# Optimization experiments

Measured on AMD Instinct MI355X. Metric: run time of the kernel, lower is better.

The kernel has to match this reference:

```python
import jax, jax.numpy as jnp
import numpy as np

DIM = 768
NUM_HEADS = 12
HEAD_DIM = DIM // NUM_HEADS
EPS = 1e-5


def layer_norm(x, w, b):
    mu = jnp.mean(x, axis=-1, keepdims=True)
    var = jnp.var(x, axis=-1, keepdims=True)
    return (x - mu) * jax.lax.rsqrt(var + EPS) * w + b


def setup_inputs() -> dict:
    key = jax.random.key(0)
    k1, k2, k3, k4, k5, k6, k7 = jax.random.split(key, 7)
    B, N = 8, 1024
    QKV = jax.random.normal(k1, (B, N, 3 * DIM), dtype=jnp.float32)
    q_norm_w = jnp.ones((HEAD_DIM,), jnp.float32)
    q_norm_b = jnp.zeros((HEAD_DIM,), jnp.float32)
    k_norm_w = jnp.ones((HEAD_DIM,), jnp.float32)
    k_norm_b = jnp.zeros((HEAD_DIM,), jnp.float32)
    lim = 1.0 / np.sqrt(DIM)
    proj_w = jax.random.uniform(k2, (DIM, DIM), jnp.float32, -lim, lim)
    proj_b = jax.random.uniform(k3, (DIM,), jnp.float32, -lim, lim)
    return {
        "QKV": QKV,
        "q_norm_w": q_norm_w, "q_norm_b": q_norm_b,
        "k_norm_w": k_norm_w, "k_norm_b": k_norm_b,
        "proj_w": proj_w, "proj_b": proj_b,
    }


def reference(QKV, q_norm_w, q_norm_b, k_norm_w, k_norm_b, proj_w, proj_b):
    B, N, C = QKV.shape
    # (B,N,3,H,D) -> (3,B,H,N,D)
    qkv = QKV.reshape(B, N, 3, NUM_HEADS, HEAD_DIM).transpose(2, 0, 3, 1, 4)
    q, k, v = qkv[0], qkv[1], qkv[2]
    q = layer_norm(q, q_norm_w, q_norm_b)
    k = layer_norm(k, k_norm_w, k_norm_b)
    scale = HEAD_DIM ** (-0.5)
    attn = jnp.einsum('bhnd,bhmd->bhnm', q, k) * scale
    attn = jax.nn.softmax(attn, axis=-1)
    x = jnp.einsum('bhnm,bhmd->bhnd', attn, v)
    x = x.transpose(0, 2, 1, 3).reshape(B, N, DIM)
    # torch Linear: x @ W^T + b
    return jnp.einsum('bnc,dc->bnd', x, proj_w) + proj_b
```

## Files before the change

kernel.cpp:

```cpp
#include <hip/hip_runtime.h>
#include <hip/hip_bf16.h>

#define DIM 768
#define NH 12
#define HD 64
#define B_ 8
#define N_ 1024
#define BH (B_*NH)
#define EPS 1e-5f
#define QSCALE 0.18033688011112042f
#define SMAX 12.0f

typedef short s16x8 __attribute__((ext_vector_type(8)));
typedef float f32x4 __attribute__((ext_vector_type(4)));

__device__ __forceinline__ unsigned pk2bf(float a, float b) {
    __hip_bfloat162 h = __float22bfloat162_rn(float2{a, b});
    union { __hip_bfloat162 h; unsigned u; } cv; cv.h = h;
    return cv.u;
}

__device__ __forceinline__ float fexp2(float x) {
#if __has_builtin(__builtin_amdgcn_exp2f)
    return __builtin_amdgcn_exp2f(x);
#else
    return exp2f(x);
#endif
}

__device__ __forceinline__ void async_cp16(const void* g, void* l) {
    __builtin_amdgcn_global_load_lds(
        (const __attribute__((address_space(1))) unsigned*)g,
        (__attribute__((address_space(3))) unsigned*)l, 16, 0, 0);
}

__global__ __launch_bounds__(256)
void ln_pack_kernel(const float* __restrict__ QKV,
                    const float* __restrict__ qw, const float* __restrict__ qb,
                    const float* __restrict__ kw, const float* __restrict__ kb,
                    unsigned short* __restrict__ Qp,
                    unsigned short* __restrict__ Kp,
                    unsigned short* __restrict__ Vp) {
    int bid = blockIdx.x;
    int bh = bid >> 4, nt = bid & 15;
    int b = bh / NH, h = bh % NH;
    int tid = threadIdx.x, w = tid >> 6, ln = tid & 63;
    int rl = w * 16 + (ln >> 2);
    int part = ln & 3;
    int n = nt * 64 + rl;

    __shared__ __attribute__((aligned(16))) unsigned short vlds[64][72];

    size_t base = ((size_t)(b * N_ + n)) * (3 * DIM) + h * HD + part * 16;
    float4 q[4], k[4], v[4];
    #pragma unroll
    for (int i = 0; i < 4; i++) {
        q[i] = *(const float4*)(QKV + base + i * 4);
        k[i] = *(const float4*)(QKV + base + DIM + i * 4);
        v[i] = *(const float4*)(QKV + base + 2 * DIM + i * 4);
    }

    float s1 = 0.f, s2 = 0.f, t1 = 0.f, t2 = 0.f;
    #pragma unroll
    for (int i = 0; i < 4; i++) {
        s1 += (q[i].x + q[i].y) + (q[i].z + q[i].w);
        s2 += (q[i].x * q[i].x + q[i].y * q[i].y) + (q[i].z * q[i].z + q[i].w * q[i].w);
        t1 += (k[i].x + k[i].y) + (k[i].z + k[i].w);
        t2 += (k[i].x * k[i].x + k[i].y * k[i].y) + (k[i].z * k[i].z + k[i].w * k[i].w);
    }
    #pragma unroll
    for (int m = 1; m < 4; m <<= 1) {
        s1 += __shfl_xor(s1, m, 64);
        s2 += __shfl_xor(s2, m, 64);
        t1 += __shfl_xor(t1, m, 64);
        t2 += __shfl_xor(t2, m, 64);
    }

    int ch = part >> 1;
    size_t tile = (((size_t)bh * 64 + (n >> 4)) * 2 + ch) * 512 + (size_t)(n & 15) * 32 + (part & 1) * 16;

    {
        float mu = s1 * (1.0f / 64.0f);
        float var = s2 * (1.0f / 64.0f) - mu * mu;
        float rstd = rsqrtf(var + EPS);
        s16x8 c0, c1;
        #pragma unroll
        for (int i = 0; i < 4; i++) {
            const float4 wv = *(const float4*)(qw + part * 16 + i * 4);
            const float4 bv = *(const float4*)(qb + part * 16 + i * 4);
            float a0 = ((q[i].x - mu) * rstd * wv.x + bv.x) * QSCALE;
            float a1 = ((q[i].y - mu) * rstd * wv.y + bv.y) * QSCALE;
            float a2 = ((q[i].z - mu) * rstd * wv.z + bv.z) * QSCALE;
            float a3 = ((q[i].w - mu) * rstd * wv.w + bv.w) * QSCALE;
            unsigned u0 = pk2bf(a0, a1), u1 = pk2bf(a2, a3);
            if (i < 2) { ((unsigned*)&c0)[i * 2] = u0; ((unsigned*)&c0)[i * 2 + 1] = u1; }
            else       { ((unsigned*)&c1)[(i - 2) * 2] = u0; ((unsigned*)&c1)[(i - 2) * 2 + 1] = u1; }
        }
        *(s16x8*)(Qp + tile) = c0;
        *(s16x8*)(Qp + tile + 8) = c1;
    }
    {
        float mu = t1 * (1.0f / 64.0f);
        float var = t2 * (1.0f / 64.0f) - mu * mu;
        float rstd = rsqrtf(var + EPS);
        s16x8 c0, c1;
        #pragma unroll
        for (int i = 0; i < 4; i++) {
            const float4 wv = *(const float4*)(kw + part * 16 + i * 4);
            const float4 bv = *(const float4*)(kb + part * 16 + i * 4);
            float a0 = (k[i].x - mu) * rstd * wv.x + bv.x;
            float a1 = (k[i].y - mu) * rstd * wv.y + bv.y;
            float a2 = (k[i].z - mu) * rstd * wv.z + bv.z;
            float a3 = (k[i].w - mu) * rstd * wv.w + bv.w;
            unsigned u0 = pk2bf(a0, a1), u1 = pk2bf(a2, a3);
            if (i < 2) { ((unsigned*)&c0)[i * 2] = u0; ((unsigned*)&c0)[i * 2 + 1] = u1; }
            else       { ((unsigned*)&c1)[(i - 2) * 2] = u0; ((unsigned*)&c1)[(i - 2) * 2 + 1] = u1; }
        }
        *(s16x8*)(Kp + tile) = c0;
        *(s16x8*)(Kp + tile + 8) = c1;
    }
    {
        s16x8 c0, c1;
        #pragma unroll
        for (int i = 0; i < 4; i++) {
            unsigned u0 = pk2bf(v[i].x, v[i].y), u1 = pk2bf(v[i].z, v[i].w);
            if (i < 2) { ((unsigned*)&c0)[i * 2] = u0; ((unsigned*)&c0)[i * 2 + 1] = u1; }
            else       { ((unsigned*)&c1)[(i - 2) * 2] = u0; ((unsigned*)&c1)[(i - 2) * 2 + 1] = u1; }
        }
        *(s16x8*)&vlds[rl][part * 16] = c0;
        *(s16x8*)&vlds[rl][part * 16 + 8] = c1;
    }
    __syncthreads();
    #pragma unroll
    for (int cc = 0; cc < 2; cc++) {
        int c = tid * 2 + cc;
        int pq = c & 3, d = (c >> 2) & 63, nb = c >> 8;
        s16x8 o;
        #pragma unroll
        for (int jj = 0; jj < 4; jj++) {
            o[jj]     = (short)vlds[nb * 32 + pq * 4 + jj][d];
            o[4 + jj] = (short)vlds[nb * 32 + 16 + pq * 4 + jj][d];
        }
        size_t off = (((size_t)bh * 32 + nt * 2 + nb) * 64 + d) * 32 + pq * 8;
        *(s16x8*)(Vp + off) = o;
    }
}

__global__ __launch_bounds__(256)
void cvt_kernel(const float* __restrict__ in, unsigned short* __restrict__ outp, int n4) {
    int i = blockIdx.x * 256 + threadIdx.x;
    if (i < n4) {
        float4 f = *(const float4*)(in + (size_t)i * 4);
        uint2 u; u.x = pk2bf(f.x, f.y); u.y = pk2bf(f.z, f.w);
        *(uint2*)(outp + (size_t)i * 4) = u;
    }
}

__global__ __launch_bounds__(256, 3)
void attn_kernel(const unsigned short* __restrict__ Qp,
                 const unsigned short* __restrict__ Kp,
                 const unsigned short* __restrict__ Vp,
                 unsigned short* __restrict__ Xb) {
    int bid = blockIdx.x;
    int bh = bid % BH;
    int mt = bid / BH;
    int b = bh / NH, h = bh % NH;
    int tid = threadIdx.x;
    int w = tid >> 6, ln = tid & 63;
    int l16 = ln & 15, quad = ln >> 4;

    __shared__ __attribute__((aligned(16))) unsigned short Ol[4][16][72];

    const unsigned short* Qb = Qp + (size_t)bh * 65536;
    const unsigned short* Kb = Kp + (size_t)bh * 65536;
    const unsigned short* Vb = Vp + (size_t)bh * 65536;

    int m0 = mt * 128 + w * 32;
    int koff = l16 * 32 + quad * 8;

    s16x8 qf[2][2];
    #pragma unroll
    for (int si = 0; si < 2; si++)
        #pragma unroll
        for (int ch = 0; ch < 2; ch++)
            qf[si][ch] = *(const s16x8*)(Qb + (size_t)(((mt * 8 + w * 2 + si) * 2 + ch)) * 512 + koff);

    f32x4 o[2][4];
    float lp[2] = {0.f, 0.f};
    #pragma unroll
    for (int si = 0; si < 2; si++)
        #pragma unroll
        for (int t = 0; t < 4; t++) o[si][t] = (f32x4){0.f, 0.f, 0.f, 0.f};

    s16x8 kfA[2][2], vfA[4], kfB[2][2], vfB[4];

#define LOADK(dst, nn)                                                          \
    _Pragma("unroll") for (int kh = 0; kh < 2; kh++)                            \
        _Pragma("unroll") for (int ch = 0; ch < 2; ch++)                        \
            dst[kh][ch] = *(const s16x8*)(Kb + (size_t)(((((nn) >> 4) + kh) * 2 + ch)) * 512 + koff);
#define LOADV(dst, nn)                                                          \
    _Pragma("unroll") for (int t = 0; t < 4; t++)                               \
        dst[t] = *(const s16x8*)(Vb + (size_t)((((nn) >> 5) * 64 + t * 16 + l16)) * 32 + quad * 8);

#define PROCESS(kf, vf)                                                         \
    _Pragma("unroll") for (int si = 0; si < 2; si++) {                          \
        f32x4 st0 = (f32x4){0.f, 0.f, 0.f, 0.f};                                \
        st0 = __builtin_amdgcn_mfma_f32_16x16x32_bf16(kf[0][0], qf[si][0], st0, 0, 0, 0); \
        st0 = __builtin_amdgcn_mfma_f32_16x16x32_bf16(kf[0][1], qf[si][1], st0, 0, 0, 0); \
        f32x4 st1 = (f32x4){0.f, 0.f, 0.f, 0.f};                                \
        st1 = __builtin_amdgcn_mfma_f32_16x16x32_bf16(kf[1][0], qf[si][0], st1, 0, 0, 0); \
        st1 = __builtin_amdgcn_mfma_f32_16x16x32_bf16(kf[1][1], qf[si][1], st1, 0, 0, 0); \
        float p0 = fexp2(st0[0] - SMAX), p1 = fexp2(st0[1] - SMAX);             \
        float p2 = fexp2(st0[2] - SMAX), p3 = fexp2(st0[3] - SMAX);             \
        float p4 = fexp2(st1[0] - SMAX), p5 = fexp2(st1[1] - SMAX);             \
        float p6 = fexp2(st1[2] - SMAX), p7 = fexp2(st1[3] - SMAX);             \
        lp[si] += ((p0 + p1) + (p2 + p3)) + ((p4 + p5) + (p6 + p7));            \
        union { uint4 u; s16x8 s; } pf;                                         \
        pf.u.x = pk2bf(p0, p1); pf.u.y = pk2bf(p2, p3);                         \
        pf.u.z = pk2bf(p4, p5); pf.u.w = pk2bf(p6, p7);                         \
        _Pragma("unroll") for (int t = 0; t < 4; t++)                           \
            o[si][t] = __builtin_amdgcn_mfma_f32_16x16x32_bf16(vf[t], pf.s, o[si][t], 0, 0, 0); \
    }

    LOADK(kfA, 0); LOADV(vfA, 0);
    for (int n0 = 0; n0 < N_; n0 += 64) {
        LOADK(kfB, n0 + 32); LOADV(vfB, n0 + 32);
        PROCESS(kfA, vfA);
        int nn = (n0 + 64) & (N_ - 1);
        LOADK(kfA, nn); LOADV(vfA, nn);
        PROCESS(kfB, vfB);
    }
#undef LOADK
#undef LOADV
#undef PROCESS

    #pragma unroll
    for (int si = 0; si < 2; si++) {
        float lt = lp[si];
        lt += __shfl_xor(lt, 16, 64);
        lt += __shfl_xor(lt, 32, 64);
        float inv = 1.0f / lt;
        #pragma unroll
        for (int t = 0; t < 4; t++) {
            uint2 u;
            u.x = pk2bf(o[si][t][0] * inv, o[si][t][1] * inv);
            u.y = pk2bf(o[si][t][2] * inv, o[si][t][3] * inv);
            *(uint2*)&Ol[w][l16][t * 16 + quad * 4] = u;
        }
        s16x8 r0 = *(const s16x8*)&Ol[w][l16][quad * 16];
        s16x8 r1 = *(const s16x8*)&Ol[w][l16][quad * 16 + 8];
        size_t row = (size_t)b * N_ + m0 + si * 16 + l16;
        *(s16x8*)(Xb + row * DIM + h * HD + quad * 16) = r0;
        *(s16x8*)(Xb + row * DIM + h * HD + quad * 16 + 8) = r1;
    }
}

__global__ __launch_bounds__(256)
void proj_kernel(const unsigned short* __restrict__ Xb,
                 const unsigned short* __restrict__ Wb,
                 const float* __restrict__ pb,
                 float* __restrict__ out) {
    int bid = blockIdx.x;
    int bm = bid % 64, bn = bid / 64;
    int tid = threadIdx.x, w = tid >> 6, ln = tid & 63;
    int l16 = ln & 15, quad = ln >> 4;
    int wm = w & 1, wn = w >> 1;

    __shared__ __attribute__((aligned(16))) unsigned short As[128 * 64];
    __shared__ __attribute__((aligned(16))) unsigned short Bs[64 * 64];

    int lr = ln >> 3;
    int gc = (ln & 7) ^ lr;

    const unsigned short* Ag = Xb + (size_t)(bm * 128 + w * 32 + lr) * DIM + gc * 8;
    const unsigned short* Bg = Wb + (size_t)(bn * 64 + w * 16 + lr) * DIM + gc * 8;

    f32x4 c[4][2];
    #pragma unroll
    for (int t = 0; t < 4; t++)
        #pragma unroll
        for (int u = 0; u < 2; u++) c[t][u] = (f32x4){0.f, 0.f, 0.f, 0.f};

    int sw = l16 & 7;

    for (int kk = 0; kk < DIM; kk += 64) {
        __syncthreads();
        #pragma unroll
        for (int j = 0; j < 4; j++)
            async_cp16(Ag + (size_t)j * 8 * DIM + kk, As + (w * 32 + j * 8) * 64);
        #pragma unroll
        for (int j = 0; j < 2; j++)
            async_cp16(Bg + (size_t)j * 8 * DIM + kk, Bs + (w * 16 + j * 8) * 64);
        __syncthreads();

        #pragma unroll
        for (int kh = 0; kh < 2; kh++) {
            s16x8 af[4], bf[2];
            #pragma unroll
            for (int t = 0; t < 4; t++) {
                int m = wm * 64 + t * 16 + l16;
                af[t] = *(const s16x8*)(As + m * 64 + (((kh * 4 + quad) ^ sw) * 8));
            }
            #pragma unroll
            for (int u = 0; u < 2; u++) {
                int n = wn * 32 + u * 16 + l16;
                bf[u] = *(const s16x8*)(Bs + n * 64 + (((kh * 4 + quad) ^ sw) * 8));
            }
            #pragma unroll
            for (int t = 0; t < 4; t++)
                #pragma unroll
                for (int u = 0; u < 2; u++)
                    c[t][u] = __builtin_amdgcn_mfma_f32_16x16x32_bf16(af[t], bf[u], c[t][u], 0, 0, 0);
        }
    }

    int m0 = bm * 128 + wm * 64;
    int n0 = bn * 64 + wn * 32;
    #pragma unroll
    for (int u = 0; u < 2; u++) {
        float bias = pb[n0 + u * 16 + l16];
        #pragma unroll
        for (int t = 0; t < 4; t++)
            #pragma unroll
            for (int r = 0; r < 4; r++) {
                int row = m0 + t * 16 + quad * 4 + r;
                out[(size_t)row * DIM + n0 + u * 16 + l16] = c[t][u][r] + bias;
            }
    }
}

extern "C" void kernel_launch(void* const* d_in, const int* in_sizes, int n_in,
                              void* d_out, int out_size, void* d_ws, size_t ws_size,
                              hipStream_t stream) {
    const float* QKV = (const float*)d_in[0];
    const float* qw  = (const float*)d_in[1];
    const float* qb  = (const float*)d_in[2];
    const float* kw  = (const float*)d_in[3];
    const float* kb  = (const float*)d_in[4];
    const float* pw  = (const float*)d_in[5];
    const float* pb  = (const float*)d_in[6];
    float* out = (float*)d_out;

    unsigned short* Qp = (unsigned short*)d_ws;
    unsigned short* Kp = Qp + (size_t)BH * 65536;
    unsigned short* Vp = Kp + (size_t)BH * 65536;
    unsigned short* Xb = Vp + (size_t)BH * 65536;
    unsigned short* Wb = Xb + (size_t)B_ * N_ * DIM;

    ln_pack_kernel<<<BH * 16, 256, 0, stream>>>(QKV, qw, qb, kw, kb, Qp, Kp, Vp);
    cvt_kernel<<<(DIM * DIM / 4 + 255) / 256, 256, 0, stream>>>(pw, Wb, DIM * DIM / 4);
    attn_kernel<<<BH * 8, 256, 0, stream>>>(Qp, Kp, Vp, Xb);
    proj_kernel<<<64 * 12, 256, 0, stream>>>(Xb, Wb, pb, out);
}
```

Before: 198.5 us.

## Stage K/V tiles in shared memory and compute softmax row sums via MFMA

Instead of every wave loading its own copy of each K/V tile from global memory into registers, the four waves split the work of copying a 64-key K/V tile into double-buffered shared memory with async copies. All waves then read their fragments from shared memory. This cuts redundant global/L2 traffic and adds a block barrier per tile. The softmax denominator now comes from an extra MFMA against a vector of ones, replacing the scalar adds and cross-lane shuffles. The constant max-subtraction before exp2 is also dropped, which relies on the normalized Q·K scores staying small enough not to overflow.

```diff
diff --git a/kernel.cpp b/kernel.cpp
--- a/kernel.cpp
+++ b/kernel.cpp
@@ -9,7 +9,6 @@
 #define BH (B_*NH)
 #define EPS 1e-5f
 #define QSCALE 0.18033688011112042f
-#define SMAX 12.0f
 
 typedef short s16x8 __attribute__((ext_vector_type(8)));
 typedef float f32x4 __attribute__((ext_vector_type(4)));
@@ -169,7 +168,8 @@
     int w = tid >> 6, ln = tid & 63;
     int l16 = ln & 15, quad = ln >> 4;
 
-    __shared__ __attribute__((aligned(16))) unsigned short Ol[4][16][72];
+    __shared__ __attribute__((aligned(16))) unsigned short Sh[2][8192];
+    unsigned short (*Ol)[16][72] = (unsigned short (*)[16][72])&Sh[0][0];
 
     const unsigned short* Qb = Qp + (size_t)bh * 65536;
     const unsigned short* Kb = Kp + (size_t)bh * 65536;
@@ -183,63 +183,82 @@
     for (int si = 0; si < 2; si++)
         #pragma unroll
         for (int ch = 0; ch < 2; ch++)
-            qf[si][ch] = *(const s16x8*)(Qb + (size_t)(((mt * 8 + w * 2 + si) * 2 + ch)) * 512 + koff);
-
-    f32x4 o[2][4];
-    float lp[2] = {0.f, 0.f};
-    #pragma unroll
-    for (int si = 0; si < 2; si++)
+            qf[si][ch] = *(const s16x8*)(Qb + (size_t)((mt * 8 + w * 2 + si) * 2 + ch) * 512 + koff);
+
+    const s16x8 ones = {0x3F80, 0x3F80, 0x3F80, 0x3F80, 0x3F80, 0x3F80, 0x3F80, 0x3F80};
+
+    f32x4 o[2][4], o4[2];
+    #pragma unroll
+    for (int si = 0; si < 2; si++) {
         #pragma unroll
         for (int t = 0; t < 4; t++) o[si][t] = (f32x4){0.f, 0.f, 0.f, 0.f};
-
-    s16x8 kfA[2][2], vfA[4], kfB[2][2], vfB[4];
-
-#define LOADK(dst, nn)                                                          \
-    _Pragma("unroll") for (int kh = 0; kh < 2; kh++)                            \
-        _Pragma("unroll") for (int ch = 0; ch < 2; ch++)                        \
-            dst[kh][ch] = *(const s16x8*)(Kb + (size_t)(((((nn) >> 4) + kh) * 2 + ch)) * 512 + koff);
-#define LOADV(dst, nn)                                                          \
-    _Pragma("unroll") for (int t = 0; t < 4; t++)                               \
-        dst[t] = *(const s16x8*)(Vb + (size_t)((((nn) >> 5) * 64 + t * 16 + l16)) * 32 + quad * 8);
-
-#define PROCESS(kf, vf)                                                         \
-    _Pragma("unroll") for (int si = 0; si < 2; si++) {                          \
-        f32x4 st0 = (f32x4){0.f, 0.f, 0.f, 0.f};                                \
-        st0 = __builtin_amdgcn_mfma_f32_16x16x32_bf16(kf[0][0], qf[si][0], st0, 0, 0, 0); \
-        st0 = __builtin_amdgcn_mfma_f32_16x16x32_bf16(kf[0][1], qf[si][1], st0, 0, 0, 0); \
-        f32x4 st1 = (f32x4){0.f, 0.f, 0.f, 0.f};                                \
-        st1 = __builtin_amdgcn_mfma_f32_16x16x32_bf16(kf[1][0], qf[si][0], st1, 0, 0, 0); \
-        st1 = __builtin_amdgcn_mfma_f32_16x16x32_bf16(kf[1][1], qf[si][1], st1, 0, 0, 0); \
-        float p0 = fexp2(st0[0] - SMAX), p1 = fexp2(st0[1] - SMAX);             \
-        float p2 = fexp2(st0[2] - SMAX), p3 = fexp2(st0[3] - SMAX);             \
-        float p4 = fexp2(st1[0] - SMAX), p5 = fexp2(st1[1] - SMAX);             \
-        float p6 = fexp2(st1[2] - SMAX), p7 = fexp2(st1[3] - SMAX);             \
-        lp[si] += ((p0 + p1) + (p2 + p3)) + ((p4 + p5) + (p6 + p7));            \
-        union { uint4 u; s16x8 s; } pf;                                         \
-        pf.u.x = pk2bf(p0, p1); pf.u.y = pk2bf(p2, p3);                         \
-        pf.u.z = pk2bf(p4, p5); pf.u.w = pk2bf(p6, p7);                         \
-        _Pragma("unroll") for (int t = 0; t < 4; t++)                           \
-            o[si][t] = __builtin_amdgcn_mfma_f32_16x16x32_bf16(vf[t], pf.s, o[si][t], 0, 0, 0); \
-    }
-
-    LOADK(kfA, 0); LOADV(vfA, 0);
+        o4[si] = (f32x4){0.f, 0.f, 0.f, 0.f};
+    }
+
+#define STAGE(s, n0)                                                            \
+    {                                                                           \
+        if (w < 2) {                                                            \
+            const unsigned short* g = Kb + (size_t)((n0) >> 4) * 1024 + (size_t)w * 2048 + ln * 8; \
+            _Pragma("unroll") for (int j = 0; j < 4; j++)                       \
+                async_cp16(g + j * 512, &Sh[s][w * 2048 + j * 512]);            \
+        } else {                                                                \
+            const unsigned short* g = Vb + (size_t)((n0) >> 5) * 2048 + (size_t)(w - 2) * 2048 + ln * 8; \
+            _Pragma("unroll") for (int j = 0; j < 4; j++)                       \
+                async_cp16(g + j * 512, &Sh[s][4096 + (w - 2) * 2048 + j * 512]); \
+        }                                                                       \
+    }
+
+    STAGE(0, 0);
     for (int n0 = 0; n0 < N_; n0 += 64) {
-        LOADK(kfB, n0 + 32); LOADV(vfB, n0 + 32);
-        PROCESS(kfA, vfA);
-        int nn = (n0 + 64) & (N_ - 1);
-        LOADK(kfA, nn); LOADV(vfA, nn);
-        PROCESS(kfB, vfB);
-    }
-#undef LOADK
-#undef LOADV
-#undef PROCESS
-
+        int cur = (n0 >> 6) & 1;
+        __syncthreads();
+        if (n0 + 64 < N_) STAGE(cur ^ 1, n0 + 64);
+
+        const unsigned short* Ks = &Sh[cur][0];
+        const unsigned short* Vs = &Sh[cur][4096];
+        #pragma unroll
+        for (int h2 = 0; h2 < 2; h2++) {
+            s16x8 kf[2][2];
+            #pragma unroll
+            for (int kh = 0; kh < 2; kh++)
+                #pragma unroll
+                for (int ch = 0; ch < 2; ch++)
+                    kf[kh][ch] = *(const s16x8*)(Ks + ((h2 * 2 + kh) * 2 + ch) * 512 + koff);
+            s16x8 vf[4];
+            #pragma unroll
+            for (int t = 0; t < 4; t++)
+                vf[t] = *(const s16x8*)(Vs + h2 * 2048 + (t * 16 + l16) * 32 + quad * 8);
+
+            #pragma unroll
+            for (int si = 0; si < 2; si++) {
+                f32x4 st0 = (f32x4){0.f, 0.f, 0.f, 0.f};
+                st0 = __builtin_amdgcn_mfma_f32_16x16x32_bf16(kf[0][0], qf[si][0], st0, 0, 0, 0);
+                st0 = __builtin_amdgcn_mfma_f32_16x16x32_bf16(kf[0][1], qf[si][1], st0, 0, 0, 0);
+                f32x4 st1 = (f32x4){0.f, 0.f, 0.f, 0.f};
+                st1 = __builtin_amdgcn_mfma_f32_16x16x32_bf16(kf[1][0], qf[si][0], st1, 0, 0, 0);
+                st1 = __builtin_amdgcn_mfma_f32_16x16x32_bf16(kf[1][1], qf[si][1], st1, 0, 0, 0);
+
+                float p0 = fexp2(st0[0]), p1 = fexp2(st0[1]);
+                float p2 = fexp2(st0[2]), p3 = fexp2(st0[3]);
+                float p4 = fexp2(st1[0]), p5 = fexp2(st1[1]);
+                float p6 = fexp2(st1[2]), p7 = fexp2(st1[3]);
+                union { uint4 u; s16x8 s; } pf;
+                pf.u.x = pk2bf(p0, p1); pf.u.y = pk2bf(p2, p3);
+                pf.u.z = pk2bf(p4, p5); pf.u.w = pk2bf(p6, p7);
+
+                #pragma unroll
+                for (int t = 0; t < 4; t++)
+                    o[si][t] = __builtin_amdgcn_mfma_f32_16x16x32_bf16(vf[t], pf.s, o[si][t], 0, 0, 0);
+                o4[si] = __builtin_amdgcn_mfma_f32_16x16x32_bf16(ones, pf.s, o4[si], 0, 0, 0);
+            }
+        }
+    }
+#undef STAGE
+
+    __syncthreads();
     #pragma unroll
     for (int si = 0; si < 2; si++) {
-        float lt = lp[si];
-        lt += __shfl_xor(lt, 16, 64);
-        lt += __shfl_xor(lt, 32, 64);
-        float inv = 1.0f / lt;
+        float inv = 1.0f / o4[si][0];
         #pragma unroll
         for (int t = 0; t < 4; t++) {
             uint2 u;
```

Result: faster. 182.5 us (-8.0%).
